# Kernel optimization log

Hardware: AMD Instinct MI355X
Metric: run time of the kernel (lower is better)

## Reference

```python
import jax, jax.numpy as jnp
import numpy as np

EOS_VALUE = 0
PAD_VALUE = 8192
EPS = 1e-08
B, T, V = 64, 64, 8192  # V == PAD_VALUE by construction of the module


def setup_inputs() -> dict:
    key = jax.random.key(0)
    k1, k2 = jax.random.split(key)
    logits = jax.random.normal(k1, (B, T, V), dtype=jnp.float32)
    targets = jax.random.randint(k2, (B, T), 0, PAD_VALUE + 1, dtype=jnp.int64)
    return {"logits": logits, "targets": targets}


def _knn_cross_entropy(xs, ys, eps):
    # xs: [B, N, D] points in prob space; ys: [B, M, D]
    # distance(i, j) = -sum_d xs[i, d] * log(clip(ys[j, d]))  (all-pairs, then per-i min)
    nb_dim = xs.shape[2]
    soft_ys = jnp.clip(ys, eps, 1.0 - (nb_dim - 1) * eps)
    # [B, N, M] pairwise cross-entropy distances (single big GEMM)
    dist = -jnp.einsum("bnd,bmd->bnm", xs, jnp.log(soft_ys))
    return dist.min(axis=-1).sum()


def reference(logits, targets):
    probs = jax.nn.softmax(logits, axis=-1)              # [B, T, V]
    eos_probs = probs[:, :, EOS_VALUE]                   # [B, T]
    eos_pos = targets == EOS_VALUE
    eos_head = (targets != PAD_VALUE) & (targets != EOS_VALUE)
    eos_target = ~eos_head

    mask = eos_head.astype(probs.dtype)[..., None]       # [B, T, 1]
    probs_m = probs * mask
    # one_hot(num_classes=pad+1), drop last (pad) and first (eos) classes -> [B, T, V-1]
    one_hot = jax.nn.one_hot(targets, PAD_VALUE + 1, dtype=probs.dtype)[:, :, 1:-1] * mask

    xs = probs_m[:, :, 1:]                               # [B, T, V-1]
    label_loss = _knn_cross_entropy(one_hot, xs, EPS) + _knn_cross_entropy(xs, one_hot, EPS)

    # BCELoss(reduction='none') on eos head
    et = eos_target.astype(probs.dtype)
    bce = -(et * jnp.log(eos_probs) + (1.0 - et) * jnp.log(1.0 - eos_probs))  # [B, T]
    ep = eos_pos.astype(probs.dtype)
    eh = eos_head.astype(probs.dtype)
    eos_loss = (
        0.5 * (bce * ep).sum(axis=1) / (ep.sum(axis=1) + EPS)
        + 0.5 * (bce * eh).sum(axis=1) / (eh.sum(axis=1) + EPS)
    ).mean()

    return label_loss, eos_loss
```

## Files before the change

### kernel.cpp

```cpp
#include <hip/hip_runtime.h>
#include <math.h>

#define B_ 64
#define T_ 64
#define V_ 8192

#define L0_ (-18.420680743952367f)
#define L1_ (-8.190335e-05f)
#define HI_ (0.99991810f)
#define EPS_ (1e-8f)

#define OFF_T2 262144
#define OFF_BA 266240
#define OFF_BH 270336

__device__ __forceinline__ float waveReduceMax(float v) {
    #pragma unroll
    for (int off = 32; off; off >>= 1) v = fmaxf(v, __shfl_xor(v, off));
    return v;
}
__device__ __forceinline__ float waveReduceSum(float v) {
    #pragma unroll
    for (int off = 32; off; off >>= 1) v += __shfl_xor(v, off);
    return v;
}

__global__ __launch_bounds__(256) void k_row(const float* __restrict__ logits,
                                             const int* __restrict__ targets,
                                             float* __restrict__ wsf,
                                             float* __restrict__ out) {
    const int tid  = threadIdx.x;
    const int wid  = tid >> 6;
    const int lane = tid & 63;
    const int row  = (blockIdx.x << 2) + wid;
    const int b    = row >> 6;
    const int n    = row & 63;
    if (row == 0 && lane < 2) out[lane] = 0.0f;

    const float4* rp4 = (const float4*)(logits + (size_t)row * V_);

    float s0 = 0.0f, s1 = 0.0f, s2 = 0.0f, s3 = 0.0f;
    #pragma unroll
    for (int k = 0; k < 8; ++k) {
        const float4 a = rp4[lane + ((k * 4 + 0) << 6)];
        const float4 c = rp4[lane + ((k * 4 + 1) << 6)];
        const float4 d = rp4[lane + ((k * 4 + 2) << 6)];
        const float4 e = rp4[lane + ((k * 4 + 3) << 6)];
        s0 += __expf(a.x) + __expf(a.y) + __expf(a.z) + __expf(a.w);
        s1 += __expf(c.x) + __expf(c.y) + __expf(c.z) + __expf(c.w);
        s2 += __expf(d.x) + __expf(d.y) + __expf(d.z) + __expf(d.w);
        s3 += __expf(e.x) + __expf(e.y) + __expf(e.z) + __expf(e.w);
    }
    const float Z = waveReduceSum((s0 + s1) + (s2 + s3));

    const float iZ = 1.0f / Z;
    const float p0 = __expf(logits[(size_t)row * V_]) * iZ;

    const int  j      = lane;
    const int  tj     = targets[b * 64 + j];
    const bool headj  = (tj != 0) && (tj != 8192);
    const int  tn     = __shfl(tj, n);
    const bool head_n = (tn != 0) && (tn != 8192);
    const bool isz_n  = (tn == 0);

    float pj = 0.0f;
    if (head_n && headj)
        pj = __expf(logits[(size_t)row * V_ + tj]) * iZ;
    wsf[(size_t)row * 64 + j] = pj;

    const float rm = waveReduceMax(pj);
    if (j == 0) {
        wsf[OFF_T2 + row] = head_n ? ((-L0_) * (1.0f - p0) - (L1_ - L0_) * rm) : 0.0f;
        wsf[OFF_BA + row] = isz_n  ? -__logf(p0)        : 0.0f;
        wsf[OFF_BH + row] = head_n ? -__logf(1.0f - p0) : 0.0f;
    }
}

__global__ __launch_bounds__(256) void k_batch(const int* __restrict__ targets,
                                               const float* __restrict__ wsf,
                                               float* __restrict__ out) {
    const int b   = blockIdx.x;
    const int tid = threadIdx.x;
    const int j   = tid & 63, g = tid >> 6;

    const float* Pb = wsf + (size_t)b * 64 * 64;
    float cm = 0.0f;
    #pragma unroll
    for (int nn = 0; nn < 16; ++nn)
        cm = fmaxf(cm, Pb[(g * 16 + nn) * 64 + j]);

    __shared__ float scm[256];
    scm[tid] = cm;
    __syncthreads();

    if (tid >= 64) return;
    const float cmj = fmaxf(fmaxf(scm[j], scm[64 + j]),
                            fmaxf(scm[128 + j], scm[192 + j]));
    const int  tj    = targets[b * 64 + j];
    const bool headj = (tj != 0) && (tj != 8192);

    float t1 = headj ? -__logf(fminf(fmaxf(cmj, EPS_), HI_)) : 0.0f;
    float lab = t1 + wsf[OFF_T2 + b * 64 + j];
    float a   = wsf[OFF_BA + b * 64 + j];
    float h   = wsf[OFF_BH + b * 64 + j];
    float cz  = (tj == 0) ? 1.0f : 0.0f;
    float ch  = headj     ? 1.0f : 0.0f;

    lab = waveReduceSum(lab);
    a   = waveReduceSum(a);
    h   = waveReduceSum(h);
    cz  = waveReduceSum(cz);
    ch  = waveReduceSum(ch);
    if (tid == 0) {
        atomicAdd(&out[0], lab);
        atomicAdd(&out[1], (0.5f * a / (cz + EPS_) + 0.5f * h / (ch + EPS_)) * (1.0f / 64.0f));
    }
}

extern "C" void kernel_launch(void* const* d_in, const int* in_sizes, int n_in,
                              void* d_out, int out_size, void* d_ws, size_t ws_size,
                              hipStream_t stream) {
    const float* logits  = (const float*)d_in[0];
    const int*   targets = (const int*)d_in[1];
    float* out = (float*)d_out;
    float* wsf = (float*)d_ws;

    k_row<<<dim3(B_ * T_ / 4), dim3(256), 0, stream>>>(logits, targets, wsf, out);
    k_batch<<<dim3(B_), dim3(256), 0, stream>>>(targets, wsf, out);
}
```

Baseline: 31.27 us.

## Move target-probability gathers from row kernel into batch kernel, store only row sums

```diff
diff --git a/kernel.cpp b/kernel.cpp
--- a/kernel.cpp
+++ b/kernel.cpp
@@ -9,10 +9,6 @@
 #define L1_ (-8.190335e-05f)
 #define HI_ (0.99991810f)
 #define EPS_ (1e-8f)
-
-#define OFF_T2 262144
-#define OFF_BA 266240
-#define OFF_BH 270336
 
 __device__ __forceinline__ float waveReduceMax(float v) {
     #pragma unroll
@@ -26,15 +22,12 @@
 }
 
 __global__ __launch_bounds__(256) void k_row(const float* __restrict__ logits,
-                                             const int* __restrict__ targets,
-                                             float* __restrict__ wsf,
+                                             float* __restrict__ Zv,
                                              float* __restrict__ out) {
     const int tid  = threadIdx.x;
     const int wid  = tid >> 6;
     const int lane = tid & 63;
     const int row  = (blockIdx.x << 2) + wid;
-    const int b    = row >> 6;
-    const int n    = row & 63;
     if (row == 0 && lane < 2) out[lane] = 0.0f;
 
     const float4* rp4 = (const float4*)(logits + (size_t)row * V_);
@@ -51,69 +44,62 @@
         s2 += __expf(d.x) + __expf(d.y) + __expf(d.z) + __expf(d.w);
         s3 += __expf(e.x) + __expf(e.y) + __expf(e.z) + __expf(e.w);
     }
-    const float Z = waveReduceSum((s0 + s1) + (s2 + s3));
-
-    const float iZ = 1.0f / Z;
-    const float p0 = __expf(logits[(size_t)row * V_]) * iZ;
-
-    const int  j      = lane;
-    const int  tj     = targets[b * 64 + j];
-    const bool headj  = (tj != 0) && (tj != 8192);
-    const int  tn     = __shfl(tj, n);
-    const bool head_n = (tn != 0) && (tn != 8192);
-    const bool isz_n  = (tn == 0);
-
-    float pj = 0.0f;
-    if (head_n && headj)
-        pj = __expf(logits[(size_t)row * V_ + tj]) * iZ;
-    wsf[(size_t)row * 64 + j] = pj;
-
-    const float rm = waveReduceMax(pj);
-    if (j == 0) {
-        wsf[OFF_T2 + row] = head_n ? ((-L0_) * (1.0f - p0) - (L1_ - L0_) * rm) : 0.0f;
-        wsf[OFF_BA + row] = isz_n  ? -__logf(p0)        : 0.0f;
-        wsf[OFF_BH + row] = head_n ? -__logf(1.0f - p0) : 0.0f;
-    }
+    const float z = waveReduceSum((s0 + s1) + (s2 + s3));
+    if (lane == 0) Zv[row] = z;
 }
 
-__global__ __launch_bounds__(256) void k_batch(const int* __restrict__ targets,
-                                               const float* __restrict__ wsf,
+__global__ __launch_bounds__(256) void k_batch(const float* __restrict__ logits,
+                                               const int* __restrict__ targets,
+                                               const float* __restrict__ Zv,
                                                float* __restrict__ out) {
-    const int b   = blockIdx.x;
-    const int tid = threadIdx.x;
-    const int j   = tid & 63, g = tid >> 6;
+    const int b    = blockIdx.x;
+    const int tid  = threadIdx.x;
+    const int wid  = tid >> 6;
+    const int lane = tid & 63;
 
-    const float* Pb = wsf + (size_t)b * 64 * 64;
+    const int  tj    = targets[b * 64 + lane];
+    const bool headj = (tj != 0) && (tj != 8192);
+
+    __shared__ float s_cm[4][64];
+    __shared__ float s_rm[64];
+
     float cm = 0.0f;
     #pragma unroll
-    for (int nn = 0; nn < 16; ++nn)
-        cm = fmaxf(cm, Pb[(g * 16 + nn) * 64 + j]);
-
-    __shared__ float scm[256];
-    scm[tid] = cm;
+    for (int r = 0; r < 16; ++r) {
+        const int n   = wid * 16 + r;
+        const int row = b * 64 + n;
+        const int tn  = __shfl(tj, n);
+        const bool head_n = (tn != 0) && (tn != 8192);
+        float pj = 0.0f;
+        if (head_n && headj)
+            pj = __expf(logits[(size_t)row * V_ + tj]) / Zv[row];
+        cm = fmaxf(cm, pj);
+        const float rm = waveReduceMax(pj);
+        if (lane == 0) s_rm[n] = rm;
+    }
+    s_cm[wid][lane] = cm;
     __syncthreads();
 
-    if (tid >= 64) return;
-    const float cmj = fmaxf(fmaxf(scm[j], scm[64 + j]),
-                            fmaxf(scm[128 + j], scm[192 + j]));
-    const int  tj    = targets[b * 64 + j];
-    const bool headj = (tj != 0) && (tj != 8192);
+    if (wid != 0) return;
+    const bool isz_n = (tj == 0);
+    const float iZ = 1.0f / Zv[b * 64 + lane];
+    const float p0 = __expf(logits[(size_t)(b * 64 + lane) * V_]) * iZ;
 
-    float t1 = headj ? -__logf(fminf(fmaxf(cmj, EPS_), HI_)) : 0.0f;
-    float lab = t1 + wsf[OFF_T2 + b * 64 + j];
-    float a   = wsf[OFF_BA + b * 64 + j];
-    float h   = wsf[OFF_BH + b * 64 + j];
-    float cz  = (tj == 0) ? 1.0f : 0.0f;
-    float ch  = headj     ? 1.0f : 0.0f;
+    const float cmj = fmaxf(fmaxf(s_cm[0][lane], s_cm[1][lane]),
+                            fmaxf(s_cm[2][lane], s_cm[3][lane]));
+    float lab = headj ? -__logf(fminf(fmaxf(cmj, EPS_), HI_)) : 0.0f;
+    if (headj) lab += (-L0_) * (1.0f - p0) - (L1_ - L0_) * s_rm[lane];
+    const float aA = isz_n ? -__logf(p0)        : 0.0f;
+    const float aH = headj ? -__logf(1.0f - p0) : 0.0f;
+    const float ca = (float)__popcll(__ballot(isz_n));
+    const float ch = (float)__popcll(__ballot(headj));
 
-    lab = waveReduceSum(lab);
-    a   = waveReduceSum(a);
-    h   = waveReduceSum(h);
-    cz  = waveReduceSum(cz);
-    ch  = waveReduceSum(ch);
-    if (tid == 0) {
-        atomicAdd(&out[0], lab);
-        atomicAdd(&out[1], (0.5f * a / (cz + EPS_) + 0.5f * h / (ch + EPS_)) * (1.0f / 64.0f));
+    const float labS = waveReduceSum(lab);
+    const float aAS  = waveReduceSum(aA);
+    const float aHS  = waveReduceSum(aH);
+    if (lane == 0) {
+        atomicAdd(&out[0], labS);
+        atomicAdd(&out[1], (0.5f * aAS / (ca + EPS_) + 0.5f * aHS / (ch + EPS_)) * (1.0f / 64.0f));
     }
 }
 
@@ -123,8 +109,8 @@
     const float* logits  = (const float*)d_in[0];
     const int*   targets = (const int*)d_in[1];
     float* out = (float*)d_out;
-    float* wsf = (float*)d_ws;
+    float* Zv  = (float*)d_ws;
 
-    k_row<<<dim3(B_ * T_ / 4), dim3(256), 0, stream>>>(logits, targets, wsf, out);
-    k_batch<<<dim3(B_), dim3(256), 0, stream>>>(targets, wsf, out);
+    k_row<<<dim3(B_ * T_ / 4), dim3(256), 0, stream>>>(logits, Zv, out);
+    k_batch<<<dim3(B_), dim3(256), 0, stream>>>(logits, targets, Zv, out);
 }
```

New measurement: 38.33 us. +22.6%, slower.

## Stream logits rows through LDS via async global_load_lds with staged waitcnt

Applied to the files above, without the earlier changes.

```diff
diff --git a/kernel.cpp b/kernel.cpp
--- a/kernel.cpp
+++ b/kernel.cpp
@@ -14,6 +14,18 @@
 #define OFF_BA 266240
 #define OFF_BH 270336
 
+template <int N>
+__device__ __forceinline__ void waitvm() {
+    __builtin_amdgcn_s_waitcnt(0xF70 + N);
+    __builtin_amdgcn_sched_barrier(0);
+}
+
+__device__ __forceinline__ void dma16(const float* g, float* l) {
+    __builtin_amdgcn_global_load_lds(
+        (const __attribute__((address_space(1))) unsigned int*)g,
+        (__attribute__((address_space(3))) unsigned int*)l, 16, 0, 0);
+}
+
 __device__ __forceinline__ float waveReduceMax(float v) {
     #pragma unroll
     for (int off = 32; off; off >>= 1) v = fmaxf(v, __shfl_xor(v, off));
@@ -29,6 +41,7 @@
                                              const int* __restrict__ targets,
                                              float* __restrict__ wsf,
                                              float* __restrict__ out) {
+    __shared__ float lds[4][4096];
     const int tid  = threadIdx.x;
     const int wid  = tid >> 6;
     const int lane = tid & 63;
@@ -37,20 +50,39 @@
     const int n    = row & 63;
     if (row == 0 && lane < 2) out[lane] = 0.0f;
 
-    const float4* rp4 = (const float4*)(logits + (size_t)row * V_);
+    const float* rowp = logits + (size_t)row * V_;
+    float* ldsw = lds[wid];
+
+    #pragma unroll
+    for (int i = 0; i < 8; ++i) dma16(rowp +        i * 256 + lane * 4, ldsw +        i * 256);
+    #pragma unroll
+    for (int i = 0; i < 8; ++i) dma16(rowp + 2048 + i * 256 + lane * 4, ldsw + 2048 + i * 256);
 
     float s0 = 0.0f, s1 = 0.0f, s2 = 0.0f, s3 = 0.0f;
+
+    #define STEP(WN, OFF) {                                             \
+        waitvm<WN>();                                                   \
+        const float4 t = *(const float4*)(ldsw + (OFF) + lane * 4);     \
+        s0 += __expf(t.x); s1 += __expf(t.y);                           \
+        s2 += __expf(t.z); s3 += __expf(t.w);                           \
+    }
+
+    STEP(15, 0 * 256)  STEP(14, 1 * 256)  STEP(13, 2 * 256)  STEP(12, 3 * 256)
+    STEP(11, 4 * 256)  STEP(10, 5 * 256)  STEP(9,  6 * 256)  STEP(8,  7 * 256)
     #pragma unroll
-    for (int k = 0; k < 8; ++k) {
-        const float4 a = rp4[lane + ((k * 4 + 0) << 6)];
-        const float4 c = rp4[lane + ((k * 4 + 1) << 6)];
-        const float4 d = rp4[lane + ((k * 4 + 2) << 6)];
-        const float4 e = rp4[lane + ((k * 4 + 3) << 6)];
-        s0 += __expf(a.x) + __expf(a.y) + __expf(a.z) + __expf(a.w);
-        s1 += __expf(c.x) + __expf(c.y) + __expf(c.z) + __expf(c.w);
-        s2 += __expf(d.x) + __expf(d.y) + __expf(d.z) + __expf(d.w);
-        s3 += __expf(e.x) + __expf(e.y) + __expf(e.z) + __expf(e.w);
-    }
+    for (int i = 0; i < 8; ++i) dma16(rowp + 4096 + i * 256 + lane * 4, ldsw + i * 256);
+
+    STEP(15, 2048 + 0 * 256)  STEP(14, 2048 + 1 * 256)  STEP(13, 2048 + 2 * 256)  STEP(12, 2048 + 3 * 256)
+    STEP(11, 2048 + 4 * 256)  STEP(10, 2048 + 5 * 256)  STEP(9,  2048 + 6 * 256)  STEP(8,  2048 + 7 * 256)
+    #pragma unroll
+    for (int i = 0; i < 8; ++i) dma16(rowp + 6144 + i * 256 + lane * 4, ldsw + 2048 + i * 256);
+
+    STEP(15, 0 * 256)  STEP(14, 1 * 256)  STEP(13, 2 * 256)  STEP(12, 3 * 256)
+    STEP(11, 4 * 256)  STEP(10, 5 * 256)  STEP(9,  6 * 256)  STEP(8,  7 * 256)
+    STEP(7, 2048 + 0 * 256)  STEP(6, 2048 + 1 * 256)  STEP(5, 2048 + 2 * 256)  STEP(4, 2048 + 3 * 256)
+    STEP(3, 2048 + 4 * 256)  STEP(2, 2048 + 5 * 256)  STEP(1, 2048 + 6 * 256)  STEP(0, 2048 + 7 * 256)
+    #undef STEP
+
     const float Z = waveReduceSum((s0 + s1) + (s2 + s3));
 
     const float iZ = 1.0f / Z;
```

Result: slower. 32.58 us (+4.2%).
